# Kernel tuning notes

Measured on AMD Instinct MI355X. Metric: run time of the kernel, lower is better.

## Reference

```python
import jax, jax.numpy as jnp
import numpy as np

DIM = 1024
NUM_HEADS = 16
DH = DIM // NUM_HEADS  # 64
B, S = 4, 2048


def setup_inputs() -> dict:
    key = jax.random.key(0)
    ks = jax.random.split(key, 9)
    sc = 0.02
    x = jax.random.normal(ks[0], (B, S, DIM), dtype=jnp.float32)
    # per-head projection weights stacked: [H, DIM, DH] (input-major layout)
    Wq = jax.random.normal(ks[1], (NUM_HEADS, DIM, DH), dtype=jnp.float32) * sc
    Wk = jax.random.normal(ks[2], (NUM_HEADS, DIM, DH), dtype=jnp.float32) * sc
    Wv = jax.random.normal(ks[3], (NUM_HEADS, DIM, DH), dtype=jnp.float32) * sc
    bq = jax.random.normal(ks[4], (NUM_HEADS, DH), dtype=jnp.float32) * sc
    bk = jax.random.normal(ks[5], (NUM_HEADS, DH), dtype=jnp.float32) * sc
    bv = jax.random.normal(ks[6], (NUM_HEADS, DH), dtype=jnp.float32) * sc
    Wo = jax.random.normal(ks[7], (DIM, DIM), dtype=jnp.float32) * sc  # (in, out)
    bo = jax.random.normal(ks[8], (DIM,), dtype=jnp.float32) * sc
    return {"x": x, "Wq": Wq, "Wk": Wk, "Wv": Wv,
            "bq": bq, "bk": bk, "bv": bv, "Wo": Wo, "bo": bo}


def reference(x, Wq, Wk, Wv, bq, bk, bv, Wo, bo):
    # Per-head Linear projections, vectorized over heads: [B,H,S,DH]
    q = jnp.einsum('bsd,hde->bhse', x, Wq) + bq[None, :, None, :]
    k = jnp.einsum('bsd,hde->bhse', x, Wk) + bk[None, :, None, :]
    v = jnp.einsum('bsd,hde->bhse', x, Wv) + bv[None, :, None, :]
    # attention_matmul: Q @ K^T normalized by sqrt(dim_per_head)
    scale = 1.0 / jnp.sqrt(jnp.asarray(DH, dtype=x.dtype))
    scores = jnp.einsum('bhse,bhte->bhst', q, k) * scale  # [B,H,S,S]
    attn = jax.nn.softmax(scores, axis=-1)
    # attn_drop with p=0.0 is identity
    o = jnp.einsum('bhst,bhte->bhse', attn, v)  # [B,H,S,DH]
    # concat along last dim in head order -> [B,S,H*DH]
    o = jnp.transpose(o, (0, 2, 1, 3)).reshape(x.shape[0], x.shape[1], NUM_HEADS * DH)
    # output projection (proj_drop p=0.0 is identity)
    return o @ Wo + bo
```

## Files before the change

### kernel.cpp

```cpp
#include <hip/hip_runtime.h>
#include <stdint.h>

#define DIM 1024
#define NH 16
#define DH 64
#define BATCH 4
#define SEQ 2048
#define MROWS (BATCH*SEQ)

typedef _Float16 half8 __attribute__((ext_vector_type(8)));
typedef __fp16 fp16x2 __attribute__((ext_vector_type(2)));
typedef float f32x4 __attribute__((ext_vector_type(4)));

__device__ __forceinline__ unsigned short f2h(float f) {
    union { _Float16 h; unsigned short u; } c; c.h = (_Float16)f; return c.u;
}
__device__ __forceinline__ unsigned int pk2u(float a, float b) {
    union { fp16x2 h; unsigned int u; } c;
    c.h = __builtin_amdgcn_cvt_pkrtz(a, b);
    return c.u;
}
__device__ __forceinline__ float fexp2(float x) {
    return __builtin_amdgcn_exp2f(x);
}
__device__ __forceinline__ void gl_lds16(const unsigned short* g, unsigned short* l) {
    __builtin_amdgcn_global_load_lds(
        (__attribute__((address_space(1))) void*)(void*)g,
        (__attribute__((address_space(3))) void*)(void*)l,
        16, 0, 0);
}


__global__ void cast_x_kernel(const float* __restrict__ x,
                              unsigned short* __restrict__ xh, int n4) {
    int i = blockIdx.x * blockDim.x + threadIdx.x;
    if (i >= n4) return;
    float4 v = reinterpret_cast<const float4*>(x)[i];
    uint2 o;
    o.x = pk2u(v.x, v.y);
    o.y = pk2u(v.z, v.w);
    reinterpret_cast<uint2*>(xh)[i] = o;
}

__global__ __launch_bounds__(256) void prep_wqkv_kernel(
    const float* __restrict__ Wq, const float* __restrict__ Wk,
    const float* __restrict__ Wv, unsigned short* __restrict__ wt)
{
    __shared__ unsigned short tile[64][65];
    const int d0 = blockIdx.x * 64;
    const int h = blockIdx.y;
    const int mat = blockIdx.z;
    const float* W = (mat == 0) ? Wq : ((mat == 1) ? Wk : Wv);
    const int c = threadIdx.x & 63;
    const int rr = threadIdx.x >> 6;
#pragma unroll
    for (int p = 0; p < 16; p++) {
        int dl = p * 4 + rr;
        tile[dl][c] = f2h(W[((size_t)h * 1024 + d0 + dl) * 64 + c]);
    }
    __syncthreads();
#pragma unroll
    for (int p = 0; p < 16; p++) {
        int el = p * 4 + rr;
        wt[(((size_t)(mat * NH + h) * 64) + el) * DIM + d0 + c] = tile[c][el];
    }
}

__global__ __launch_bounds__(256) void prep_wo_kernel(
    const float* __restrict__ Wo, unsigned short* __restrict__ wot)
{
    __shared__ unsigned short tile[64][65];
    const int d0 = blockIdx.x * 64;
    const int o0 = blockIdx.y * 64;
    const int c = threadIdx.x & 63;
    const int rr = threadIdx.x >> 6;
#pragma unroll
    for (int p = 0; p < 16; p++) {
        int dl = p * 4 + rr;
        tile[dl][c] = f2h(Wo[(size_t)(d0 + dl) * DIM + o0 + c]);
    }
    __syncthreads();
#pragma unroll
    for (int p = 0; p < 16; p++) {
        int ol = p * 4 + rr;
        wot[(size_t)(o0 + ol) * DIM + d0 + c] = tile[c][ol];
    }
}

__global__ __launch_bounds__(256) void transpose_v_kernel(
    const unsigned short* __restrict__ Vb, unsigned short* __restrict__ Vt)
{
    __shared__ unsigned short tile[64][65];
    const int s0 = blockIdx.x * 64;
    const size_t bh = (size_t)blockIdx.z * NH + blockIdx.y;
    const int c = threadIdx.x & 63;
    const int rr = threadIdx.x >> 6;
    const unsigned short* src = Vb + bh * SEQ * DH;
    unsigned short* dst = Vt + bh * DH * SEQ;
#pragma unroll
    for (int p = 0; p < 16; p++) {
        int sl = p * 4 + rr;
        tile[sl][c] = src[(size_t)(s0 + sl) * DH + c];
    }
    __syncthreads();
#pragma unroll
    for (int p = 0; p < 16; p++) {
        int dr = p * 4 + rr;
        dst[(size_t)dr * SEQ + s0 + c] = tile[c][dr];
    }
}

__global__ __launch_bounds__(256) void qkv_gemm_kernel(
    const unsigned short* __restrict__ xh,
    const unsigned short* __restrict__ wt,
    const float* __restrict__ bq, const float* __restrict__ bk,
    const float* __restrict__ bv,
    unsigned short* __restrict__ Qb,
    unsigned short* __restrict__ Kb,
    unsigned short* __restrict__ Vb)
{
    const int rowblk = blockIdx.x;
    const int hpair = blockIdx.y;
    const int mat = blockIdx.z;
    const int wave = threadIdx.x >> 6;
    const int lane = threadIdx.x & 63;
    const int quad = lane >> 4;
    const int lr = lane & 15;
    const int mhalf = wave & 1;
    const int nhalf = wave >> 1;

    __shared__ __align__(16) unsigned short Ab[2][128 * 32];
    __shared__ __align__(16) unsigned short Bt[2][128 * 32];

    const unsigned short* Asrc = xh + (size_t)rowblk * 128 * DIM;
    const unsigned short* Bsrc = wt + (size_t)(mat * NH + hpair * 2) * DH * DIM;

    const int srow = lane >> 2;
    const int scs = lane & 3;

    f32x4 acc[4][4];
#pragma unroll
    for (int mt = 0; mt < 4; mt++)
#pragma unroll
        for (int nt = 0; nt < 4; nt++) acc[mt][nt] = (f32x4){0.f, 0.f, 0.f, 0.f};

    auto stage = [&](int k0, int sel) {
#pragma unroll
        for (int jj = 0; jj < 2; jj++) {
            const int j = wave * 2 + jj;
            const int r = j * 16 + srow;
            const int cg = scs ^ ((r >> 1) & 3);
            gl_lds16(Asrc + (size_t)r * DIM + k0 + cg * 8, &Ab[sel][j * 512]);
            gl_lds16(Bsrc + (size_t)r * DIM + k0 + cg * 8, &Bt[sel][j * 512]);
        }
    };

    stage(0, 0);
    __syncthreads();

    for (int i = 0; i < DIM / 32; i++) {
        const int sel = i & 1;
        if (i + 1 < DIM / 32) stage((i + 1) * 32, sel ^ 1);

        half8 af[4], bf[4];
#pragma unroll
        for (int mt = 0; mt < 4; mt++) {
            const int row = mhalf * 64 + mt * 16 + lr;
            const int slot = quad ^ ((row >> 1) & 3);
            af[mt] = *reinterpret_cast<const half8*>(&Ab[sel][row * 32 + slot * 8]);
        }
#pragma unroll
        for (int nt = 0; nt < 4; nt++) {
            const int row = nhalf * 64 + nt * 16 + lr;
            const int slot = quad ^ ((row >> 1) & 3);
            bf[nt] = *reinterpret_cast<const half8*>(&Bt[sel][row * 32 + slot * 8]);
        }
#pragma unroll
        for (int mt = 0; mt < 4; mt++)
#pragma unroll
            for (int nt = 0; nt < 4; nt++)
                acc[mt][nt] = __builtin_amdgcn_mfma_f32_16x16x32_f16(
                    af[mt], bf[nt], acc[mt][nt], 0, 0, 0);
        __syncthreads();
    }

    const float* bias = (mat == 0) ? bq : ((mat == 1) ? bk : bv);
    const float scale = (mat == 0) ? 0.1803368801111601f : 1.0f;
    unsigned short* outp = (mat == 0) ? Qb : ((mat == 1) ? Kb : Vb);
    const int rowBase = rowblk * 128 + mhalf * 64;
    const int bb = rowBase / SEQ;
    const int sBase = rowBase % SEQ;

#pragma unroll
    for (int mt = 0; mt < 4; mt++) {
        const int s0 = sBase + mt * 16 + quad * 4;
#pragma unroll
        for (int nt = 0; nt < 4; nt++) {
            const int e = nhalf * 64 + nt * 16 + lr;
            const int head = hpair * 2 + (e >> 6);
            const int n = e & 63;
            const float bvl = bias[head * DH + n];
            const size_t base = (size_t)(bb * NH + head) * SEQ * DH;
#pragma unroll
            for (int r = 0; r < 4; r++) {
                outp[base + (size_t)(s0 + r) * DH + n] = f2h((acc[mt][nt][r] + bvl) * scale);
            }
        }
    }
}

__global__ __launch_bounds__(256) void attn_kernel(
    const unsigned short* __restrict__ Qb,
    const unsigned short* __restrict__ Kb,
    const unsigned short* __restrict__ Vt,
    unsigned short* __restrict__ Ob)
{
    const int h = blockIdx.y;
    const int bb = blockIdx.z;
    const int wave = threadIdx.x >> 6;
    const int lane = threadIdx.x & 63;
    const int quad = lane >> 4;
    const int lr = lane & 15;
    const int qBase = blockIdx.x * 128 + wave * 32;

    const size_t bh = (size_t)(bb * NH + h);
    const unsigned short* Qh = Qb + bh * SEQ * DH;
    const unsigned short* Kh = Kb + bh * SEQ * DH;
    const unsigned short* Vh = Vt + bh * DH * SEQ;

    __shared__ __align__(16) unsigned short Kbuf[2][64 * 64];
    __shared__ __align__(16) unsigned short Vbuf[2][64 * 64];
    __shared__ __align__(16) unsigned short Pall[4][32 * 72];
    unsigned short* Pw = Pall[wave];

    const int srow = lane >> 3;
    const int scs = lane & 7;
    const int cg = scs ^ srow;
    int koff[2], voff[2];
#pragma unroll
    for (int jj = 0; jj < 2; jj++) {
        const int r = wave * 16 + jj * 8 + srow;
        koff[jj] = r * DH + cg * 8;
        voff[jj] = r * SEQ + cg * 8;
    }

    auto stage = [&](int kt, int sel) {
        gl_lds16(Kh + (size_t)kt * DH + koff[0], &Kbuf[sel][wave * 1024]);
        gl_lds16(Kh + (size_t)kt * DH + koff[1], &Kbuf[sel][wave * 1024 + 512]);
        gl_lds16(Vh + kt + voff[0], &Vbuf[sel][wave * 1024]);
        gl_lds16(Vh + kt + voff[1], &Vbuf[sel][wave * 1024 + 512]);
    };

    half8 qf[2][2];
#pragma unroll
    for (int mt = 0; mt < 2; mt++)
#pragma unroll
        for (int kc = 0; kc < 2; kc++)
            qf[mt][kc] = *reinterpret_cast<const half8*>(
                Qh + (size_t)(qBase + mt * 16 + lr) * DH + kc * 32 + quad * 8);

    const f32x4 zf = {0.f, 0.f, 0.f, 0.f};
    f32x4 o[4][2];
    float lsum[2] = {0.f, 0.f};
#pragma unroll
    for (int t = 0; t < 4; t++)
#pragma unroll
        for (int mt = 0; mt < 2; mt++) o[t][mt] = zf;

    auto compute = [&](int sel) {
        f32x4 sacc[4][2];
#pragma unroll
        for (int kc = 0; kc < 2; kc++) {
            half8 kf[4];
#pragma unroll
            for (int t = 0; t < 4; t++) {
                const int row = t * 16 + lr;
                const int slot = (kc * 4 + quad) ^ (row & 7);
                kf[t] = *reinterpret_cast<const half8*>(&Kbuf[sel][row * 64 + slot * 8]);
            }
#pragma unroll
            for (int t = 0; t < 4; t++)
#pragma unroll
                for (int mt = 0; mt < 2; mt++)
                    sacc[t][mt] = __builtin_amdgcn_mfma_f32_16x16x32_f16(
                        kf[t], qf[mt][kc], kc ? sacc[t][mt] : zf, 0, 0, 0);
        }

#pragma unroll
        for (int t = 0; t < 4; t++)
#pragma unroll
            for (int mt = 0; mt < 2; mt++) {
                float p0 = fexp2(sacc[t][mt][0]);
                float p1 = fexp2(sacc[t][mt][1]);
                float p2 = fexp2(sacc[t][mt][2]);
                float p3 = fexp2(sacc[t][mt][3]);
                lsum[mt] += (p0 + p1) + (p2 + p3);
                uint2 w;
                w.x = pk2u(p0, p1);
                w.y = pk2u(p2, p3);
                *reinterpret_cast<uint2*>(&Pw[(mt * 16 + lr) * 72 + t * 16 + quad * 4]) = w;
            }

#pragma unroll
        for (int kc = 0; kc < 2; kc++) {
            half8 pf[2];
#pragma unroll
            for (int mt = 0; mt < 2; mt++)
                pf[mt] = *reinterpret_cast<const half8*>(
                    &Pw[(mt * 16 + lr) * 72 + kc * 32 + quad * 8]);
            half8 vf[4];
#pragma unroll
            for (int t = 0; t < 4; t++) {
                const int row = t * 16 + lr;
                const int slot = (kc * 4 + quad) ^ (row & 7);
                vf[t] = *reinterpret_cast<const half8*>(&Vbuf[sel][row * 64 + slot * 8]);
            }
#pragma unroll
            for (int t = 0; t < 4; t++)
#pragma unroll
                for (int mt = 0; mt < 2; mt++)
                    o[t][mt] = __builtin_amdgcn_mfma_f32_16x16x32_f16(
                        vf[t], pf[mt], o[t][mt], 0, 0, 0);
        }
    };

    stage(0, 0);
    __syncthreads();

    for (int i = 0; i < SEQ / 64; i += 2) {
        stage((i + 1) * 64, 1);
        compute(0);
        __syncthreads();
        if (i + 2 < SEQ / 64) stage((i + 2) * 64, 0);
        compute(1);
        __syncthreads();
    }

    float inv[2];
#pragma unroll
    for (int mt = 0; mt < 2; mt++) {
        float l = lsum[mt];
        l += __shfl_xor(l, 16);
        l += __shfl_xor(l, 32);
        inv[mt] = 1.f / l;
    }
#pragma unroll
    for (int t = 0; t < 4; t++)
#pragma unroll
        for (int mt = 0; mt < 2; mt++) {
            uint2 pkd;
            pkd.x = pk2u(o[t][mt][0] * inv[mt], o[t][mt][1] * inv[mt]);
            pkd.y = pk2u(o[t][mt][2] * inv[mt], o[t][mt][3] * inv[mt]);
            const int q = qBase + mt * 16 + lr;
            *reinterpret_cast<uint2*>(
                Ob + ((size_t)(bb * SEQ + q)) * DIM + h * DH + t * 16 + quad * 4) = pkd;
        }
}

__global__ __launch_bounds__(256) void out_proj_kernel(
    const unsigned short* __restrict__ Ob,
    const unsigned short* __restrict__ wot,
    const float* __restrict__ bo,
    float* __restrict__ out)
{
    const int rowblk = blockIdx.x;
    const int colblk = blockIdx.y;
    const int wave = threadIdx.x >> 6;
    const int lane = threadIdx.x & 63;
    const int quad = lane >> 4;
    const int lr = lane & 15;
    const int mhalf = wave & 1;
    const int nhalf = wave >> 1;

    __shared__ __align__(16) unsigned short Ab[2][128 * 32];
    __shared__ __align__(16) unsigned short Bt[2][128 * 32];

    const unsigned short* Asrc = Ob + (size_t)rowblk * 128 * DIM;
    const unsigned short* Bsrc = wot + (size_t)colblk * 128 * DIM;

    const int srow = lane >> 2;
    const int scs = lane & 3;

    f32x4 acc[4][4];
#pragma unroll
    for (int mt = 0; mt < 4; mt++)
#pragma unroll
        for (int nt = 0; nt < 4; nt++) acc[mt][nt] = (f32x4){0.f, 0.f, 0.f, 0.f};

    auto stage = [&](int k0, int sel) {
#pragma unroll
        for (int jj = 0; jj < 2; jj++) {
            const int j = wave * 2 + jj;
            const int r = j * 16 + srow;
            const int cg = scs ^ ((r >> 1) & 3);
            gl_lds16(Asrc + (size_t)r * DIM + k0 + cg * 8, &Ab[sel][j * 512]);
            gl_lds16(Bsrc + (size_t)r * DIM + k0 + cg * 8, &Bt[sel][j * 512]);
        }
    };

    stage(0, 0);
    __syncthreads();

    for (int i = 0; i < DIM / 32; i++) {
        const int sel = i & 1;
        if (i + 1 < DIM / 32) stage((i + 1) * 32, sel ^ 1);

        half8 af[4], bf[4];
#pragma unroll
        for (int mt = 0; mt < 4; mt++) {
            const int row = mhalf * 64 + mt * 16 + lr;
            const int slot = quad ^ ((row >> 1) & 3);
            af[mt] = *reinterpret_cast<const half8*>(&Ab[sel][row * 32 + slot * 8]);
        }
#pragma unroll
        for (int nt = 0; nt < 4; nt++) {
            const int row = nhalf * 64 + nt * 16 + lr;
            const int slot = quad ^ ((row >> 1) & 3);
            bf[nt] = *reinterpret_cast<const half8*>(&Bt[sel][row * 32 + slot * 8]);
        }
#pragma unroll
        for (int mt = 0; mt < 4; mt++)
#pragma unroll
            for (int nt = 0; nt < 4; nt++)
                acc[mt][nt] = __builtin_amdgcn_mfma_f32_16x16x32_f16(
                    af[mt], bf[nt], acc[mt][nt], 0, 0, 0);
        __syncthreads();
    }

    const int rowBase = rowblk * 128 + mhalf * 64;
    const int colBase = colblk * 128 + nhalf * 64;
#pragma unroll
    for (int mt = 0; mt < 4; mt++) {
#pragma unroll
        for (int nt = 0; nt < 4; nt++) {
            const int col = colBase + nt * 16 + lr;
            const float bias = bo[col];
#pragma unroll
            for (int r = 0; r < 4; r++) {
                int row = rowBase + mt * 16 + quad * 4 + r;
                out[(size_t)row * DIM + col] = acc[mt][nt][r] + bias;
            }
        }
    }
}


extern "C" void kernel_launch(void* const* d_in, const int* in_sizes, int n_in,
                              void* d_out, int out_size, void* d_ws, size_t ws_size,
                              hipStream_t stream) {
    const float* x  = (const float*)d_in[0];
    const float* Wq = (const float*)d_in[1];
    const float* Wk = (const float*)d_in[2];
    const float* Wv = (const float*)d_in[3];
    const float* bq = (const float*)d_in[4];
    const float* bk = (const float*)d_in[5];
    const float* bv = (const float*)d_in[6];
    const float* Wo = (const float*)d_in[7];
    const float* bo = (const float*)d_in[8];
    float* out = (float*)d_out;

    unsigned short* xh  = (unsigned short*)d_ws;
    unsigned short* wt  = xh  + (size_t)MROWS * DIM;
    unsigned short* wot = wt  + (size_t)3 * NH * DH * DIM;
    unsigned short* Qb  = wot + (size_t)DIM * DIM;
    unsigned short* Kb  = Qb  + (size_t)BATCH * NH * SEQ * DH;
    unsigned short* Vb  = Kb  + (size_t)BATCH * NH * SEQ * DH;
    unsigned short* Vt  = Vb  + (size_t)BATCH * NH * SEQ * DH;
    unsigned short* Ob  = Vt  + (size_t)BATCH * NH * SEQ * DH;

    {
        int n4 = MROWS * DIM / 4;
        cast_x_kernel<<<(n4 + 255) / 256, 256, 0, stream>>>(x, xh, n4);
    }
    prep_wqkv_kernel<<<dim3(16, NH, 3), 256, 0, stream>>>(Wq, Wk, Wv, wt);
    prep_wo_kernel<<<dim3(16, 16), 256, 0, stream>>>(Wo, wot);
    qkv_gemm_kernel<<<dim3(64, 8, 3), 256, 0, stream>>>(xh, wt, bq, bk, bv, Qb, Kb, Vb);
    transpose_v_kernel<<<dim3(SEQ / 64, NH, BATCH), 256, 0, stream>>>(Vb, Vt);
    attn_kernel<<<dim3(SEQ / 128, NH, BATCH), 256, 0, stream>>>(Qb, Kb, Vt, Ob);
    out_proj_kernel<<<dim3(64, 8), 256, 0, stream>>>(Ob, wot, bo, out);
}
```

Before: 319.0 us.

## Use 32x32x16 MFMA in attention and pass P via permlane32 swap instead of LDS

Rewrites the attention inner loop to use 32x32x16 MFMA tiles instead of 16x16x32, so each wave covers its 32 query rows with a single accumulator tile. The exponentiated score tile is rearranged into B-operand layout in registers with permlane32_swap, removing the per-wave LDS round trip for P and its shared memory. It also adds s_setprio around the MFMA blocks and a 4-waves occupancy hint in launch bounds. The cost is more complex lane mapping and possible register pressure from 16-wide accumulators.

```diff
diff --git a/kernel.cpp b/kernel.cpp
--- a/kernel.cpp
+++ b/kernel.cpp
@@ -11,6 +11,8 @@
 typedef _Float16 half8 __attribute__((ext_vector_type(8)));
 typedef __fp16 fp16x2 __attribute__((ext_vector_type(2)));
 typedef float f32x4 __attribute__((ext_vector_type(4)));
+typedef float f32x16 __attribute__((ext_vector_type(16)));
+typedef unsigned int u32x2 __attribute__((ext_vector_type(2)));
 
 __device__ __forceinline__ unsigned short f2h(float f) {
     union { _Float16 h; unsigned short u; } c; c.h = (_Float16)f; return c.u;
@@ -209,7 +211,7 @@
     }
 }
 
-__global__ __launch_bounds__(256) void attn_kernel(
+__global__ __launch_bounds__(256, 4) void attn_kernel(
     const unsigned short* __restrict__ Qb,
     const unsigned short* __restrict__ Kb,
     const unsigned short* __restrict__ Vt,
@@ -219,8 +221,8 @@
     const int bb = blockIdx.z;
     const int wave = threadIdx.x >> 6;
     const int lane = threadIdx.x & 63;
-    const int quad = lane >> 4;
-    const int lr = lane & 15;
+    const int ql = lane & 31;
+    const int hi = lane >> 5;
     const int qBase = blockIdx.x * 128 + wave * 32;
 
     const size_t bh = (size_t)(bb * NH + h);
@@ -230,8 +232,6 @@
 
     __shared__ __align__(16) unsigned short Kbuf[2][64 * 64];
     __shared__ __align__(16) unsigned short Vbuf[2][64 * 64];
-    __shared__ __align__(16) unsigned short Pall[4][32 * 72];
-    unsigned short* Pw = Pall[wave];
 
     const int srow = lane >> 3;
     const int scs = lane & 7;
@@ -251,77 +251,78 @@
         gl_lds16(Vh + kt + voff[1], &Vbuf[sel][wave * 1024 + 512]);
     };
 
-    half8 qf[2][2];
-#pragma unroll
-    for (int mt = 0; mt < 2; mt++)
-#pragma unroll
-        for (int kc = 0; kc < 2; kc++)
-            qf[mt][kc] = *reinterpret_cast<const half8*>(
-                Qh + (size_t)(qBase + mt * 16 + lr) * DH + kc * 32 + quad * 8);
-
-    const f32x4 zf = {0.f, 0.f, 0.f, 0.f};
-    f32x4 o[4][2];
-    float lsum[2] = {0.f, 0.f};
-#pragma unroll
-    for (int t = 0; t < 4; t++)
-#pragma unroll
-        for (int mt = 0; mt < 2; mt++) o[t][mt] = zf;
+    half8 qf[4];
+#pragma unroll
+    for (int ks = 0; ks < 4; ks++)
+        qf[ks] = *reinterpret_cast<const half8*>(
+            Qh + (size_t)(qBase + ql) * DH + ks * 16 + hi * 8);
+
+    f32x16 z16;
+#pragma unroll
+    for (int e = 0; e < 16; e++) z16[e] = 0.f;
+
+    f32x16 o[2];
+#pragma unroll
+    for (int mt = 0; mt < 2; mt++) o[mt] = z16;
+    float lsA = 0.f, lsB = 0.f;
 
     auto compute = [&](int sel) {
-        f32x4 sacc[4][2];
-#pragma unroll
-        for (int kc = 0; kc < 2; kc++) {
-            half8 kf[4];
-#pragma unroll
-            for (int t = 0; t < 4; t++) {
-                const int row = t * 16 + lr;
-                const int slot = (kc * 4 + quad) ^ (row & 7);
-                kf[t] = *reinterpret_cast<const half8*>(&Kbuf[sel][row * 64 + slot * 8]);
-            }
-#pragma unroll
-            for (int t = 0; t < 4; t++)
-#pragma unroll
-                for (int mt = 0; mt < 2; mt++)
-                    sacc[t][mt] = __builtin_amdgcn_mfma_f32_16x16x32_f16(
-                        kf[t], qf[mt][kc], kc ? sacc[t][mt] : zf, 0, 0, 0);
-        }
-
-#pragma unroll
-        for (int t = 0; t < 4; t++)
+        f32x16 sacc[2];
+        __builtin_amdgcn_s_setprio(1);
+#pragma unroll
+        for (int ks = 0; ks < 4; ks++) {
+#pragma unroll
+            for (int kb = 0; kb < 2; kb++) {
+                const int row = kb * 32 + ql;
+                const int slot = (ks * 2 + hi) ^ (row & 7);
+                half8 kf = *reinterpret_cast<const half8*>(&Kbuf[sel][row * 64 + slot * 8]);
+                sacc[kb] = __builtin_amdgcn_mfma_f32_32x32x16_f16(
+                    kf, qf[ks], ks ? sacc[kb] : z16, 0, 0, 0);
+            }
+        }
+        __builtin_amdgcn_s_setprio(0);
+
+        unsigned int pfu[4][4];
+#pragma unroll
+        for (int kb = 0; kb < 2; kb++) {
+            unsigned int c[8];
+#pragma unroll
+            for (int m = 0; m < 8; m++) {
+                float a = fexp2(sacc[kb][2 * m]);
+                float b2 = fexp2(sacc[kb][2 * m + 1]);
+                if (m & 1) lsB += a + b2; else lsA += a + b2;
+                c[m] = pk2u(a, b2);
+            }
+#pragma unroll
+            for (int ks = 0; ks < 2; ks++) {
+                u32x2 w02 = __builtin_amdgcn_permlane32_swap(
+                    c[4 * ks + 0], c[4 * ks + 2], false, false);
+                u32x2 w13 = __builtin_amdgcn_permlane32_swap(
+                    c[4 * ks + 1], c[4 * ks + 3], false, false);
+                pfu[kb * 2 + ks][0] = w02[0];
+                pfu[kb * 2 + ks][1] = w13[0];
+                pfu[kb * 2 + ks][2] = w02[1];
+                pfu[kb * 2 + ks][3] = w13[1];
+            }
+        }
+
+        __builtin_amdgcn_s_setprio(1);
+#pragma unroll
+        for (int ks = 0; ks < 4; ks++) {
+            union { unsigned int u[4]; half8 h; } cv;
+            cv.u[0] = pfu[ks][0]; cv.u[1] = pfu[ks][1];
+            cv.u[2] = pfu[ks][2]; cv.u[3] = pfu[ks][3];
+            const half8 pf = cv.h;
 #pragma unroll
             for (int mt = 0; mt < 2; mt++) {
-                float p0 = fexp2(sacc[t][mt][0]);
-                float p1 = fexp2(sacc[t][mt][1]);
-                float p2 = fexp2(sacc[t][mt][2]);
-                float p3 = fexp2(sacc[t][mt][3]);
-                lsum[mt] += (p0 + p1) + (p2 + p3);
-                uint2 w;
-                w.x = pk2u(p0, p1);
-                w.y = pk2u(p2, p3);
-                *reinterpret_cast<uint2*>(&Pw[(mt * 16 + lr) * 72 + t * 16 + quad * 4]) = w;
-            }
-
-#pragma unroll
-        for (int kc = 0; kc < 2; kc++) {
-            half8 pf[2];
-#pragma unroll
-            for (int mt = 0; mt < 2; mt++)
-                pf[mt] = *reinterpret_cast<const half8*>(
-                    &Pw[(mt * 16 + lr) * 72 + kc * 32 + quad * 8]);
-            half8 vf[4];
-#pragma unroll
-            for (int t = 0; t < 4; t++) {
-                const int row = t * 16 + lr;
-                const int slot = (kc * 4 + quad) ^ (row & 7);
-                vf[t] = *reinterpret_cast<const half8*>(&Vbuf[sel][row * 64 + slot * 8]);
-            }
-#pragma unroll
-            for (int t = 0; t < 4; t++)
-#pragma unroll
-                for (int mt = 0; mt < 2; mt++)
-                    o[t][mt] = __builtin_amdgcn_mfma_f32_16x16x32_f16(
-                        vf[t], pf[mt], o[t][mt], 0, 0, 0);
-        }
+                const int row = mt * 32 + ql;
+                const int slot = (ks * 2 + hi) ^ (row & 7);
+                half8 vf = *reinterpret_cast<const half8*>(&Vbuf[sel][row * 64 + slot * 8]);
+                o[mt] = __builtin_amdgcn_mfma_f32_32x32x16_f16(
+                    vf, pf, o[mt], 0, 0, 0);
+            }
+        }
+        __builtin_amdgcn_s_setprio(0);
     };
 
     stage(0, 0);
@@ -336,25 +337,20 @@
         __syncthreads();
     }
 
-    float inv[2];
+    float l = lsA + lsB;
+    l += __shfl_xor(l, 32);
+    const float inv = 1.f / l;
+    const size_t orow = (size_t)(bb * SEQ + qBase + ql) * DIM + h * DH;
 #pragma unroll
     for (int mt = 0; mt < 2; mt++) {
-        float l = lsum[mt];
-        l += __shfl_xor(l, 16);
-        l += __shfl_xor(l, 32);
-        inv[mt] = 1.f / l;
-    }
-#pragma unroll
-    for (int t = 0; t < 4; t++)
-#pragma unroll
-        for (int mt = 0; mt < 2; mt++) {
+#pragma unroll
+        for (int g = 0; g < 4; g++) {
             uint2 pkd;
-            pkd.x = pk2u(o[t][mt][0] * inv[mt], o[t][mt][1] * inv[mt]);
-            pkd.y = pk2u(o[t][mt][2] * inv[mt], o[t][mt][3] * inv[mt]);
-            const int q = qBase + mt * 16 + lr;
-            *reinterpret_cast<uint2*>(
-                Ob + ((size_t)(bb * SEQ + q)) * DIM + h * DH + t * 16 + quad * 4) = pkd;
-        }
+            pkd.x = pk2u(o[mt][4 * g + 0] * inv, o[mt][4 * g + 1] * inv);
+            pkd.y = pk2u(o[mt][4 * g + 2] * inv, o[mt][4 * g + 3] * inv);
+            *reinterpret_cast<uint2*>(Ob + orow + mt * 32 + 8 * g + 4 * hi) = pkd;
+        }
+    }
 }
 
 __global__ __launch_bounds__(256) void out_proj_kernel(
```

New measurement: 310.0 us. 1.03x faster.
